# Performance work log

Hardware: AMD Instinct MI355X
Metric: run time of the kernel (lower is better)

Reference implementation:

```python
import jax, jax.numpy as jnp
import numpy as np

BN_EPS = 1e-5
DIST_MIN = 1e-8
K = 3


def setup_inputs() -> dict:
    key = jax.random.key(0)
    ks = jax.random.split(key, 6)
    B, Nl, Nh, Ch, Cl, out_ch = 4, 8192, 2048, 256, 128, 256
    in_ch = Ch + Cl
    xyz_low = jax.random.normal(ks[0], (B, Nl, 3), jnp.float32)
    xyz_high = jax.random.normal(ks[1], (B, Nh, 3), jnp.float32)
    feat_low = jax.random.normal(ks[2], (B, Cl, Nl), jnp.float32)
    feat_high = jax.random.normal(ks[3], (B, Ch, Nh), jnp.float32)
    # 1x1 Conv1d params (kernel size 1 -> plain channel-mixing matrix)
    W = jax.random.normal(ks[4], (out_ch, in_ch), jnp.float32) * (1.0 / np.sqrt(in_ch))
    b = jax.random.normal(ks[5], (out_ch,), jnp.float32) * 0.01
    gamma = jnp.ones((out_ch,), jnp.float32)
    beta = jnp.zeros((out_ch,), jnp.float32)
    return {"xyz_low": xyz_low, "xyz_high": xyz_high, "feat_low": feat_low,
            "feat_high": feat_high, "W": W, "b": b, "gamma": gamma, "beta": beta}


def reference(xyz_low, xyz_high, feat_low, feat_high, W, b, gamma, beta):
    # --- pairwise euclidean distances (B, Nl, Nh), like torch.cdist ---
    d2 = (jnp.sum(xyz_low ** 2, -1)[:, :, None]
          + jnp.sum(xyz_high ** 2, -1)[:, None, :]
          - 2.0 * jnp.einsum('bld,bhd->blh', xyz_low, xyz_high))
    d = jnp.sqrt(jnp.maximum(d2, 0.0))
    # --- 3-NN (smallest distances) ---
    _, idx = jax.lax.top_k(-d, K)                      # (B, Nl, K)
    dist = jnp.maximum(jnp.take_along_axis(d, idx, axis=-1), DIST_MIN)
    w = 1.0 / dist
    w = w / jnp.sum(w, axis=-1, keepdims=True)         # (B, Nl, K)
    # --- gather neighbor features and inverse-distance interpolate ---
    f_high_T = jnp.transpose(feat_high, (0, 2, 1))      # (B, Nh, Ch)
    neigh = jax.vmap(lambda f, i: f[i])(f_high_T, idx)  # (B, Nl, K, Ch)
    f_interp = jnp.einsum('blk,blkc->bcl', w, neigh)    # (B, Ch, Nl)
    f_cat = jnp.concatenate([f_interp, feat_low], axis=1)  # (B, Ch+Cl, Nl)
    # --- 1x1 Conv1d + BatchNorm1d (training-mode batch stats) + ReLU ---
    y = jnp.einsum('oc,bcn->bon', W, f_cat) + b[None, :, None]
    mean = jnp.mean(y, axis=(0, 2), keepdims=True)
    var = jnp.var(y, axis=(0, 2), keepdims=True)        # biased, as in torch BN
    yn = (y - mean) * jax.lax.rsqrt(var + BN_EPS)
    return jax.nn.relu(gamma[None, :, None] * yn + beta[None, :, None])
```

## Files before the change

kernel.cpp:

```cpp
#include <hip/hip_runtime.h>

constexpr int B_   = 4;
constexpr int NL   = 8192;
constexpr int NH   = 2048;
constexpr int CH   = 256;
constexpr int CL   = 128;
constexpr int CIN  = 384;
constexpr int COUT = 256;

typedef _Float16 f16;
typedef _Float16 f16x8 __attribute__((ext_vector_type(8)));
typedef float    f32x4 __attribute__((ext_vector_type(4)));

#define INS3F(d, h, B0, B1, B2, I0, I1, I2) do {                             \
    bool c0_ = (d) < (B0), c1_ = (d) < (B1), c2_ = (d) < (B2);               \
    int ni1_ = c0_ ? (I0) : (c1_ ? (h) : (I1));                              \
    int ni2_ = c1_ ? (I1) : (c2_ ? (h) : (I2));                              \
    I0 = c0_ ? (h) : (I0); I1 = ni1_; I2 = ni2_;                             \
    float nb1_ = __builtin_amdgcn_fmed3f(B0, B1, (d));                       \
    float nb2_ = __builtin_amdgcn_fmed3f(B1, B2, (d));                       \
    B0 = fminf(B0, (d)); B1 = nb1_; B2 = nb2_;                               \
} while (0)

__global__ __launch_bounds__(256) void knn_prep_kernel(
    const float* __restrict__ xyz_low, const float* __restrict__ xyz_high,
    const float* __restrict__ feat_high, const float* __restrict__ Wm,
    f16* __restrict__ fhT, f16* __restrict__ Wh,
    float* __restrict__ cdG, int* __restrict__ ciG)
{
    __shared__ __align__(16) char smraw[14080];
    const int bid = blockIdx.x, tid = threadIdx.x;

    if (bid < 2048) {
        float4*         pts = (float4*)smraw;
        float*          md  = (float*)(smraw + 4096);
        unsigned short* mi  = (unsigned short*)(smraw + 10752);
        const int tile = bid >> 3, oct = bid & 7;
        const int b = tile >> 6, l0 = (tile & 63) * 128;
        const int w = tid >> 6, p = tid & 63;
        const int hbase = oct * 256;

        const float* xh = xyz_high + ((size_t)b * NH + hbase) * 3;
        {
            const int h = tid;
            float x = xh[h * 3], yy = xh[h * 3 + 1], z = xh[h * 3 + 2];
            pts[h] = make_float4(x, yy, z, x * x + yy * yy + z * z);
        }
        __syncthreads();

        const float* xlA = xyz_low + ((size_t)b * NL + l0 + p) * 3;
        const float* xlB = xyz_low + ((size_t)b * NL + l0 + 64 + p) * 3;
        const float lxA = xlA[0], lyA = xlA[1], lzA = xlA[2];
        const float lxB = xlB[0], lyB = xlB[1], lzB = xlB[2];
        const float slA = lxA * lxA + lyA * lyA + lzA * lzA;
        const float slB = lxB * lxB + lyB * lyB + lzB * lzB;

        float a0 = 1e30f, a1 = 1e30f, a2 = 1e30f;
        float c0 = 1e30f, c1 = 1e30f, c2 = 1e30f;
        int ia0 = 0, ia1 = 0, ia2 = 0, ic0 = 0, ic1 = 0, ic2 = 0;
        const int h0 = w * 64;
        #pragma unroll 4
        for (int h = h0; h < h0 + 64; ++h) {
            float4 pt = pts[h];
            float dA = fmaf(-2.0f, fmaf(lxA, pt.x, fmaf(lyA, pt.y, lzA * pt.z)),
                            slA + pt.w);
            float dB = fmaf(-2.0f, fmaf(lxB, pt.x, fmaf(lyB, pt.y, lzB * pt.z)),
                            slB + pt.w);
            INS3F(dA, h, a0, a1, a2, ia0, ia1, ia2);
            INS3F(dB, h, c0, c1, c2, ic0, ic1, ic2);
        }
        const int cbA = p * 13 + w * 3;
        const int cbB = (p + 64) * 13 + w * 3;
        md[cbA] = a0;     mi[cbA] = (unsigned short)(hbase + ia0);
        md[cbA + 1] = a1; mi[cbA + 1] = (unsigned short)(hbase + ia1);
        md[cbA + 2] = a2; mi[cbA + 2] = (unsigned short)(hbase + ia2);
        md[cbB] = c0;     mi[cbB] = (unsigned short)(hbase + ic0);
        md[cbB + 1] = c1; mi[cbB + 1] = (unsigned short)(hbase + ic1);
        md[cbB + 2] = c2; mi[cbB + 2] = (unsigned short)(hbase + ic2);
        __syncthreads();

        if (tid < 128) {
            float e0 = 1e30f, e1 = 1e30f, e2 = 1e30f;
            int j0 = 0, j1 = 0, j2 = 0;
            #pragma unroll
            for (int q = 0; q < 12; ++q) {
                float d = md[tid * 13 + q];
                int  ii = mi[tid * 13 + q];
                INS3F(d, ii, e0, e1, e2, j0, j1, j2);
            }
            const size_t dst = (size_t)bid * 384 + tid;
            cdG[dst]       = e0; ciG[dst]       = j0;
            cdG[dst + 128] = e1; ciG[dst + 128] = j1;
            cdG[dst + 256] = e2; ciG[dst + 256] = j2;
        }
    } else if (bid < 2560) {
        float (*tt)[33] = (float(*)[33])smraw;
        const int tx = tid & 31, ty = tid >> 5;
        #pragma unroll
        for (int k = 0; k < 4; ++k) {
            const int u  = (bid - 2048) * 4 + k;
            const int ub = u >> 9, ut = u & 511;
            const int h0 = (ut & 63) * 32, c0 = (ut >> 6) * 32;
            #pragma unroll
            for (int pp = 0; pp < 4; ++pp)
                tt[ty + pp * 8][tx] =
                    feat_high[((size_t)ub * CH + c0 + ty + pp * 8) * NH + h0 + tx];
            __syncthreads();
            #pragma unroll
            for (int pp = 0; pp < 4; ++pp)
                fhT[((size_t)ub * NH + h0 + ty + pp * 8) * CH + c0 + tx] =
                    (f16)tt[tx][ty + pp * 8];
            __syncthreads();
        }
    } else {
        const int i = (bid - 2560) * 256 + tid;
        Wh[i] = (f16)Wm[i];
    }
}

__global__ __launch_bounds__(512) void gemm_kernel(
    const float* __restrict__ feat_low, const f16* __restrict__ fhT,
    const f16* __restrict__ Wh, const float* __restrict__ bias,
    const float* __restrict__ cdG, const int* __restrict__ ciG,
    f16* __restrict__ yh, float* __restrict__ ps, float* __restrict__ psq)
{
    __shared__ __align__(16) char smraw[51712];
    f16*   As   = (f16*)smraw;
    int*   idxL = (int*)(smraw + 50176);
    float* wL   = (float*)(smraw + 50944);

    const int bid = blockIdx.x, tid = threadIdx.x;
    const int b = bid >> 7, l0 = (bid & 127) * 64;
    const int lane = tid & 63, w = tid >> 6;

    if (tid < 64) {
        float e0 = 1e30f, e1 = 1e30f, e2 = 1e30f;
        int j0 = 0, j1 = 0, j2 = 0;
        const int t128 = b * 64 + ((bid & 127) >> 1);
        const int poff = (bid & 1) * 64 + tid;
        #pragma unroll
        for (int oct = 0; oct < 8; ++oct) {
            const size_t src = (size_t)(t128 * 8 + oct) * 384 + poff;
            #pragma unroll
            for (int q = 0; q < 3; ++q) {
                float d = cdG[src + q * 128];
                int  ii = ciG[src + q * 128];
                INS3F(d, ii, e0, e1, e2, j0, j1, j2);
            }
        }
        float d0 = sqrtf(fmaxf(e0, 0.0f));
        float d1 = sqrtf(fmaxf(e1, 0.0f));
        float d2f = sqrtf(fmaxf(e2, 0.0f));
        float iw0 = 1.0f / fmaxf(d0, 1e-8f);
        float iw1 = 1.0f / fmaxf(d1, 1e-8f);
        float iw2 = 1.0f / fmaxf(d2f, 1e-8f);
        float sum = iw0 + iw1 + iw2;
        idxL[tid] = j0; idxL[64 + tid] = j1; idxL[128 + tid] = j2;
        wL[tid] = iw0 / sum; wL[64 + tid] = iw1 / sum; wL[128 + tid] = iw2 / sum;
    }
    __syncthreads();

    {
        const int p = tid >> 3, q = tid & 7;
        const int j0 = idxL[p], j1 = idxL[64 + p], j2 = idxL[128 + p];
        const float u0 = wL[p], u1 = wL[64 + p], u2 = wL[128 + p];
        const f16* r0 = fhT + ((size_t)b * NH + j0) * CH + q * 32;
        const f16* r1 = fhT + ((size_t)b * NH + j1) * CH + q * 32;
        const f16* r2 = fhT + ((size_t)b * NH + j2) * CH + q * 32;
        #pragma unroll
        for (int j = 0; j < 4; ++j) {
            f16x8 v0 = *(const f16x8*)(r0 + j * 8);
            f16x8 v1 = *(const f16x8*)(r1 + j * 8);
            f16x8 v2 = *(const f16x8*)(r2 + j * 8);
            f16x8 o;
            #pragma unroll
            for (int e = 0; e < 8; ++e)
                o[e] = (f16)(u0 * (float)v0[e] + u1 * (float)v1[e]
                             + u2 * (float)v2[e]);
            *(f16x8*)&As[p * 392 + q * 32 + j * 8] = o;
        }
        const int l = tid & 63, cq = tid >> 6;
        const float* flb = feat_low + ((size_t)b * CL + cq * 16) * NL + l0 + l;
        f16 tmp[16];
        #pragma unroll
        for (int i = 0; i < 16; ++i)
            tmp[i] = (f16)flb[(size_t)i * NL];
        *(f16x8*)&As[l * 392 + 256 + cq * 16]     = *(const f16x8*)&tmp[0];
        *(f16x8*)&As[l * 392 + 256 + cq * 16 + 8] = *(const f16x8*)&tmp[8];
    }
    __syncthreads();

    f32x4 acc[2][4] = {};
    const int kb = (lane >> 4) * 8;
    const int r  = lane & 15;
    #pragma unroll
    for (int kt = 0; kt < 12; ++kt) {
        const int k0 = kt * 32;
        f16x8 a[2], bb[4];
        #pragma unroll
        for (int mi = 0; mi < 2; ++mi)
            a[mi] = *(const f16x8*)&Wh[(size_t)(w * 32 + mi * 16 + r) * CIN
                                       + k0 + kb];
        #pragma unroll
        for (int ni = 0; ni < 4; ++ni)
            bb[ni] = *(const f16x8*)&As[(ni * 16 + r) * 392 + k0 + kb];
        #pragma unroll
        for (int mi = 0; mi < 2; ++mi)
            #pragma unroll
            for (int ni = 0; ni < 4; ++ni)
                acc[mi][ni] = __builtin_amdgcn_mfma_f32_16x16x32_f16(
                    a[mi], bb[ni], acc[mi][ni], 0, 0, 0);
    }

    const int r4 = (lane >> 4) * 4, cl = lane & 15;
    #pragma unroll
    for (int mi = 0; mi < 2; ++mi) {
        #pragma unroll
        for (int j = 0; j < 4; ++j) {
            const int o = w * 32 + mi * 16 + r4 + j;
            const float bi = bias[o];
            float s = 0.0f, sq = 0.0f;
            #pragma unroll
            for (int ni = 0; ni < 4; ++ni) {
                acc[mi][ni][j] += bi;
                float v = acc[mi][ni][j];
                s += v; sq += v * v;
            }
            #pragma unroll
            for (int m = 1; m < 16; m <<= 1) {
                s  += __shfl_xor(s, m);
                sq += __shfl_xor(sq, m);
            }
            if (cl == 0) {
                ps [o * 512 + bid] = s;
                psq[o * 512 + bid] = sq;
            }
        }
    }
    __syncthreads();

    f16* Ys = (f16*)smraw;
    #pragma unroll
    for (int mi = 0; mi < 2; ++mi)
        #pragma unroll
        for (int j = 0; j < 4; ++j) {
            const int o = w * 32 + mi * 16 + r4 + j;
            #pragma unroll
            for (int ni = 0; ni < 4; ++ni)
                Ys[o * 72 + cl + ni * 16] = (f16)acc[mi][ni][j];
        }
    __syncthreads();
    {
        const int o = tid >> 1, half = tid & 1;
        f16* dst = yh + ((size_t)b * COUT + o) * NL + l0 + half * 32;
        #pragma unroll
        for (int j = 0; j < 4; ++j)
            *(f16x8*)(dst + j * 8) = *(const f16x8*)&Ys[o * 72 + half * 32 + j * 8];
    }
}

__global__ __launch_bounds__(256) void stats_apply_kernel(
    const float* __restrict__ ps, const float* __restrict__ psq,
    const f16* __restrict__ yh,
    const float* __restrict__ gamma, const float* __restrict__ beta,
    float* __restrict__ y)
{
    const int o = blockIdx.x, b = blockIdx.y, tid = threadIdx.x;
    const int w = tid >> 6, lane = tid & 63;

    float s = ps[o * 512 + tid] + ps[o * 512 + 256 + tid];
    float q = psq[o * 512 + tid] + psq[o * 512 + 256 + tid];
    #pragma unroll
    for (int m = 32; m > 0; m >>= 1) {
        s += __shfl_down(s, m);
        q += __shfl_down(q, m);
    }
    __shared__ float red[8];
    if (lane == 0) { red[w] = s; red[4 + w] = q; }
    __syncthreads();
    s = red[0] + red[1] + red[2] + red[3];
    q = red[4] + red[5] + red[6] + red[7];
    const float n  = (float)(B_ * NL);
    const float mu = s / n;
    const float rs = rsqrtf(q / n - mu * mu + 1e-5f);
    const float g  = gamma[o], be = beta[o];

    const f16* src = yh + ((size_t)b * COUT + o) * NL;
    float*     dst = y  + ((size_t)b * COUT + o) * NL;
    #pragma unroll
    for (int it = 0; it < 4; ++it) {
        const int base = it * 2048 + tid * 8;
        f16x8 v = *(const f16x8*)(src + base);
        float4 o1, o2;
        o1.x = fmaxf(fmaf(g, ((float)v[0] - mu) * rs, be), 0.0f);
        o1.y = fmaxf(fmaf(g, ((float)v[1] - mu) * rs, be), 0.0f);
        o1.z = fmaxf(fmaf(g, ((float)v[2] - mu) * rs, be), 0.0f);
        o1.w = fmaxf(fmaf(g, ((float)v[3] - mu) * rs, be), 0.0f);
        o2.x = fmaxf(fmaf(g, ((float)v[4] - mu) * rs, be), 0.0f);
        o2.y = fmaxf(fmaf(g, ((float)v[5] - mu) * rs, be), 0.0f);
        o2.z = fmaxf(fmaf(g, ((float)v[6] - mu) * rs, be), 0.0f);
        o2.w = fmaxf(fmaf(g, ((float)v[7] - mu) * rs, be), 0.0f);
        *(float4*)(dst + base)     = o1;
        *(float4*)(dst + base + 4) = o2;
    }
}

extern "C" void kernel_launch(void* const* d_in, const int* in_sizes, int n_in,
                              void* d_out, int out_size, void* d_ws, size_t ws_size,
                              hipStream_t stream)
{
    const float* xyz_low   = (const float*)d_in[0];
    const float* xyz_high  = (const float*)d_in[1];
    const float* feat_low  = (const float*)d_in[2];
    const float* feat_high = (const float*)d_in[3];
    const float* Wm        = (const float*)d_in[4];
    const float* bias      = (const float*)d_in[5];
    const float* gamma     = (const float*)d_in[6];
    const float* beta      = (const float*)d_in[7];
    float* y = (float*)d_out;

    float* ps   = (float*)d_ws;
    float* psq  = ps + (size_t)COUT * 512;
    float* cdG  = psq + (size_t)COUT * 512;
    int*   ciG  = (int*)(cdG + (size_t)2048 * 384);
    f16*   Wh   = (f16*)(ciG + (size_t)2048 * 384);
    f16*   fhT  = Wh + (size_t)COUT * CIN;
    f16*   yh   = fhT + (size_t)B_ * NH * CH;

    knn_prep_kernel<<<2944, 256, 0, stream>>>(
        xyz_low, xyz_high, feat_high, Wm, fhT, Wh, cdG, ciG);
    gemm_kernel<<<512, 512, 0, stream>>>(
        feat_low, fhT, Wh, bias, cdG, ciG, yh, ps, psq);
    stats_apply_kernel<<<dim3(COUT, B_), 256, 0, stream>>>(
        ps, psq, yh, gamma, beta, y);
}
```

Measured before the change: 78.43 us.

## Fuse 3-NN search into GEMM kernel and drop global candidate buffers

Moves the brute-force 3-nearest-neighbour search out of the prep kernel and into the GEMM kernel. Each GEMM block now stages all high-res points of its batch in shared memory. Each of its 8 waves scans a 256-point slice for the block's 64 low-res points, and the per-wave top-3 lists are merged through shared memory. This removes the global write and read of the per-octant candidate distances and indices and shrinks the prep kernel to the transpose and weight-cast work. In exchange, the GEMM kernel does the serial KNN work before its own gather and MFMA phase, with fewer waves in total available to hide that compute.

After: 75.82 us. -3.3%, faster.

```diff
diff --git a/kernel.cpp b/kernel.cpp
--- a/kernel.cpp
+++ b/kernel.cpp
@@ -22,83 +22,18 @@
     B0 = fminf(B0, (d)); B1 = nb1_; B2 = nb2_;                               \
 } while (0)
 
-__global__ __launch_bounds__(256) void knn_prep_kernel(
-    const float* __restrict__ xyz_low, const float* __restrict__ xyz_high,
+__global__ __launch_bounds__(256) void prep_kernel(
     const float* __restrict__ feat_high, const float* __restrict__ Wm,
-    f16* __restrict__ fhT, f16* __restrict__ Wh,
-    float* __restrict__ cdG, int* __restrict__ ciG)
+    f16* __restrict__ fhT, f16* __restrict__ Wh)
 {
-    __shared__ __align__(16) char smraw[14080];
+    __shared__ float tt[32][33];
     const int bid = blockIdx.x, tid = threadIdx.x;
 
-    if (bid < 2048) {
-        float4*         pts = (float4*)smraw;
-        float*          md  = (float*)(smraw + 4096);
-        unsigned short* mi  = (unsigned short*)(smraw + 10752);
-        const int tile = bid >> 3, oct = bid & 7;
-        const int b = tile >> 6, l0 = (tile & 63) * 128;
-        const int w = tid >> 6, p = tid & 63;
-        const int hbase = oct * 256;
-
-        const float* xh = xyz_high + ((size_t)b * NH + hbase) * 3;
-        {
-            const int h = tid;
-            float x = xh[h * 3], yy = xh[h * 3 + 1], z = xh[h * 3 + 2];
-            pts[h] = make_float4(x, yy, z, x * x + yy * yy + z * z);
-        }
-        __syncthreads();
-
-        const float* xlA = xyz_low + ((size_t)b * NL + l0 + p) * 3;
-        const float* xlB = xyz_low + ((size_t)b * NL + l0 + 64 + p) * 3;
-        const float lxA = xlA[0], lyA = xlA[1], lzA = xlA[2];
-        const float lxB = xlB[0], lyB = xlB[1], lzB = xlB[2];
-        const float slA = lxA * lxA + lyA * lyA + lzA * lzA;
-        const float slB = lxB * lxB + lyB * lyB + lzB * lzB;
-
-        float a0 = 1e30f, a1 = 1e30f, a2 = 1e30f;
-        float c0 = 1e30f, c1 = 1e30f, c2 = 1e30f;
-        int ia0 = 0, ia1 = 0, ia2 = 0, ic0 = 0, ic1 = 0, ic2 = 0;
-        const int h0 = w * 64;
-        #pragma unroll 4
-        for (int h = h0; h < h0 + 64; ++h) {
-            float4 pt = pts[h];
-            float dA = fmaf(-2.0f, fmaf(lxA, pt.x, fmaf(lyA, pt.y, lzA * pt.z)),
-                            slA + pt.w);
-            float dB = fmaf(-2.0f, fmaf(lxB, pt.x, fmaf(lyB, pt.y, lzB * pt.z)),
-                            slB + pt.w);
-            INS3F(dA, h, a0, a1, a2, ia0, ia1, ia2);
-            INS3F(dB, h, c0, c1, c2, ic0, ic1, ic2);
-        }
-        const int cbA = p * 13 + w * 3;
-        const int cbB = (p + 64) * 13 + w * 3;
-        md[cbA] = a0;     mi[cbA] = (unsigned short)(hbase + ia0);
-        md[cbA + 1] = a1; mi[cbA + 1] = (unsigned short)(hbase + ia1);
-        md[cbA + 2] = a2; mi[cbA + 2] = (unsigned short)(hbase + ia2);
-        md[cbB] = c0;     mi[cbB] = (unsigned short)(hbase + ic0);
-        md[cbB + 1] = c1; mi[cbB + 1] = (unsigned short)(hbase + ic1);
-        md[cbB + 2] = c2; mi[cbB + 2] = (unsigned short)(hbase + ic2);
-        __syncthreads();
-
-        if (tid < 128) {
-            float e0 = 1e30f, e1 = 1e30f, e2 = 1e30f;
-            int j0 = 0, j1 = 0, j2 = 0;
-            #pragma unroll
-            for (int q = 0; q < 12; ++q) {
-                float d = md[tid * 13 + q];
-                int  ii = mi[tid * 13 + q];
-                INS3F(d, ii, e0, e1, e2, j0, j1, j2);
-            }
-            const size_t dst = (size_t)bid * 384 + tid;
-            cdG[dst]       = e0; ciG[dst]       = j0;
-            cdG[dst + 128] = e1; ciG[dst + 128] = j1;
-            cdG[dst + 256] = e2; ciG[dst + 256] = j2;
-        }
-    } else if (bid < 2560) {
-        float (*tt)[33] = (float(*)[33])smraw;
+    if (bid < 512) {
         const int tx = tid & 31, ty = tid >> 5;
         #pragma unroll
         for (int k = 0; k < 4; ++k) {
-            const int u  = (bid - 2048) * 4 + k;
+            const int u  = bid * 4 + k;
             const int ub = u >> 9, ut = u & 511;
             const int h0 = (ut & 63) * 32, c0 = (ut >> 6) * 32;
             #pragma unroll
@@ -113,40 +48,77 @@
             __syncthreads();
         }
     } else {
-        const int i = (bid - 2560) * 256 + tid;
+        const int i = (bid - 512) * 256 + tid;
         Wh[i] = (f16)Wm[i];
     }
 }
 
 __global__ __launch_bounds__(512) void gemm_kernel(
+    const float* __restrict__ xyz_low, const float* __restrict__ xyz_high,
     const float* __restrict__ feat_low, const f16* __restrict__ fhT,
     const f16* __restrict__ Wh, const float* __restrict__ bias,
-    const float* __restrict__ cdG, const int* __restrict__ ciG,
     f16* __restrict__ yh, float* __restrict__ ps, float* __restrict__ psq)
 {
     __shared__ __align__(16) char smraw[51712];
-    f16*   As   = (f16*)smraw;
-    int*   idxL = (int*)(smraw + 50176);
-    float* wL   = (float*)(smraw + 50944);
+    f16*            As   = (f16*)smraw;
+    float4*         pts  = (float4*)smraw;
+    float*          md   = (float*)(smraw + 32768);
+    unsigned short* mi   = (unsigned short*)(smraw + 39168);
+    int*            idxL = (int*)(smraw + 50176);
+    float*          wL   = (float*)(smraw + 50944);
 
     const int bid = blockIdx.x, tid = threadIdx.x;
     const int b = bid >> 7, l0 = (bid & 127) * 64;
     const int lane = tid & 63, w = tid >> 6;
 
+    {
+        const float* xh = xyz_high + (size_t)b * NH * 3;
+        #pragma unroll
+        for (int k = 0; k < 4; ++k) {
+            const int h = k * 512 + tid;
+            float x = xh[h * 3], yy = xh[h * 3 + 1], z = xh[h * 3 + 2];
+            pts[h] = make_float4(x, yy, z, x * x + yy * yy + z * z);
+        }
+    }
+    __syncthreads();
+    {
+        const float* xl = xyz_low + ((size_t)b * NL + l0 + lane) * 3;
+        const float lx = xl[0], ly = xl[1], lz = xl[2];
+        const float sl = lx * lx + ly * ly + lz * lz;
+
+        float a0 = 1e30f, a1 = 1e30f, a2 = 1e30f;
+        float c0 = 1e30f, c1 = 1e30f, c2 = 1e30f;
+        int ia0 = 0, ia1 = 0, ia2 = 0, ic0 = 0, ic1 = 0, ic2 = 0;
+        const int hA = w * 256, hB = hA + 128;
+        #pragma unroll 4
+        for (int i = 0; i < 128; ++i) {
+            float4 pA = pts[hA + i];
+            float4 pB = pts[hB + i];
+            float dA = fmaf(-2.0f, fmaf(lx, pA.x, fmaf(ly, pA.y, lz * pA.z)),
+                            sl + pA.w);
+            float dB = fmaf(-2.0f, fmaf(lx, pB.x, fmaf(ly, pB.y, lz * pB.z)),
+                            sl + pB.w);
+            INS3F(dA, hA + i, a0, a1, a2, ia0, ia1, ia2);
+            INS3F(dB, hB + i, c0, c1, c2, ic0, ic1, ic2);
+        }
+        INS3F(c0, ic0, a0, a1, a2, ia0, ia1, ia2);
+        INS3F(c1, ic1, a0, a1, a2, ia0, ia1, ia2);
+        INS3F(c2, ic2, a0, a1, a2, ia0, ia1, ia2);
+        const int cb = lane * 25 + w * 3;
+        md[cb] = a0;     mi[cb] = (unsigned short)ia0;
+        md[cb + 1] = a1; mi[cb + 1] = (unsigned short)ia1;
+        md[cb + 2] = a2; mi[cb + 2] = (unsigned short)ia2;
+    }
+    __syncthreads();
+
     if (tid < 64) {
         float e0 = 1e30f, e1 = 1e30f, e2 = 1e30f;
         int j0 = 0, j1 = 0, j2 = 0;
-        const int t128 = b * 64 + ((bid & 127) >> 1);
-        const int poff = (bid & 1) * 64 + tid;
-        #pragma unroll
-        for (int oct = 0; oct < 8; ++oct) {
-            const size_t src = (size_t)(t128 * 8 + oct) * 384 + poff;
-            #pragma unroll
-            for (int q = 0; q < 3; ++q) {
-                float d = cdG[src + q * 128];
-                int  ii = ciG[src + q * 128];
-                INS3F(d, ii, e0, e1, e2, j0, j1, j2);
-            }
+        #pragma unroll
+        for (int q = 0; q < 24; ++q) {
+            float d = md[tid * 25 + q];
+            int  ii = mi[tid * 25 + q];
+            INS3F(d, ii, e0, e1, e2, j0, j1, j2);
         }
         float d0 = sqrtf(fmaxf(e0, 0.0f));
         float d1 = sqrtf(fmaxf(e1, 0.0f));
@@ -198,32 +170,32 @@
         const int k0 = kt * 32;
         f16x8 a[2], bb[4];
         #pragma unroll
-        for (int mi = 0; mi < 2; ++mi)
-            a[mi] = *(const f16x8*)&Wh[(size_t)(w * 32 + mi * 16 + r) * CIN
-                                       + k0 + kb];
+        for (int mi2 = 0; mi2 < 2; ++mi2)
+            a[mi2] = *(const f16x8*)&Wh[(size_t)(w * 32 + mi2 * 16 + r) * CIN
+                                        + k0 + kb];
         #pragma unroll
         for (int ni = 0; ni < 4; ++ni)
             bb[ni] = *(const f16x8*)&As[(ni * 16 + r) * 392 + k0 + kb];
         #pragma unroll
-        for (int mi = 0; mi < 2; ++mi)
+        for (int mi2 = 0; mi2 < 2; ++mi2)
             #pragma unroll
             for (int ni = 0; ni < 4; ++ni)
-                acc[mi][ni] = __builtin_amdgcn_mfma_f32_16x16x32_f16(
-                    a[mi], bb[ni], acc[mi][ni], 0, 0, 0);
+                acc[mi2][ni] = __builtin_amdgcn_mfma_f32_16x16x32_f16(
+                    a[mi2], bb[ni], acc[mi2][ni], 0, 0, 0);
     }
 
     const int r4 = (lane >> 4) * 4, cl = lane & 15;
     #pragma unroll
-    for (int mi = 0; mi < 2; ++mi) {
+    for (int mi2 = 0; mi2 < 2; ++mi2) {
         #pragma unroll
         for (int j = 0; j < 4; ++j) {
-            const int o = w * 32 + mi * 16 + r4 + j;
+            const int o = w * 32 + mi2 * 16 + r4 + j;
             const float bi = bias[o];
             float s = 0.0f, sq = 0.0f;
             #pragma unroll
             for (int ni = 0; ni < 4; ++ni) {
-                acc[mi][ni][j] += bi;
-                float v = acc[mi][ni][j];
+                acc[mi2][ni][j] += bi;
+                float v = acc[mi2][ni][j];
                 s += v; sq += v * v;
             }
             #pragma unroll
@@ -241,13 +213,13 @@
 
     f16* Ys = (f16*)smraw;
     #pragma unroll
-    for (int mi = 0; mi < 2; ++mi)
+    for (int mi2 = 0; mi2 < 2; ++mi2)
         #pragma unroll
         for (int j = 0; j < 4; ++j) {
-            const int o = w * 32 + mi * 16 + r4 + j;
+            const int o = w * 32 + mi2 * 16 + r4 + j;
             #pragma unroll
             for (int ni = 0; ni < 4; ++ni)
-                Ys[o * 72 + cl + ni * 16] = (f16)acc[mi][ni][j];
+                Ys[o * 72 + cl + ni * 16] = (f16)acc[mi2][ni][j];
         }
     __syncthreads();
     {
@@ -321,16 +293,13 @@
 
     float* ps   = (float*)d_ws;
     float* psq  = ps + (size_t)COUT * 512;
-    float* cdG  = psq + (size_t)COUT * 512;
-    int*   ciG  = (int*)(cdG + (size_t)2048 * 384);
-    f16*   Wh   = (f16*)(ciG + (size_t)2048 * 384);
+    f16*   Wh   = (f16*)(psq + (size_t)COUT * 512);
     f16*   fhT  = Wh + (size_t)COUT * CIN;
     f16*   yh   = fhT + (size_t)B_ * NH * CH;
 
-    knn_prep_kernel<<<2944, 256, 0, stream>>>(
-        xyz_low, xyz_high, feat_high, Wm, fhT, Wh, cdG, ciG);
+    prep_kernel<<<896, 256, 0, stream>>>(feat_high, Wm, fhT, Wh);
     gemm_kernel<<<512, 512, 0, stream>>>(
-        feat_low, fhT, Wh, bias, cdG, ciG, yh, ps, psq);
+        xyz_low, xyz_high, feat_low, fhT, Wh, bias, yh, ps, psq);
     stats_apply_kernel<<<dim3(COUT, B_), 256, 0, stream>>>(
         ps, psq, yh, gamma, beta, y);
 }
```
